# Kernel tuning notes

Hardware: AMD Instinct MI355X
Metric: run time of the kernel (lower is better)

The kernel has to match this reference:

```python
import jax, jax.numpy as jnp
import numpy as np


def setup_inputs() -> dict:
    key = jax.random.key(0)
    k1, k2 = jax.random.split(key)
    B, C, M, N = 4, 3, 4096, 8192
    query = jax.random.normal(k1, (B, C, M), dtype=jnp.float32)
    points = jax.random.normal(k2, (B, C, N), dtype=jnp.float32)
    return {"k": 16, "query": query, "points": points}


def reference(k, query, points):
    # query: BxCxM, points: BxCxN  (trans=True path of original module)
    q = jnp.swapaxes(query, 1, 2)   # BxMxC
    p = jnp.swapaxes(points, 1, 2)  # BxNxC
    # squared L2 distances (FAISS GpuIndexFlatL2): BxMxN
    q2 = jnp.sum(q * q, axis=-1, keepdims=True)           # BxMx1
    p2 = jnp.sum(p * p, axis=-1)[:, None, :]              # Bx1xN
    dist = q2 + p2 - 2.0 * jnp.einsum('bmc,bnc->bmn', q, p)
    # k smallest distances, sorted ascending (FAISS sorts results)
    _, index_batch = jax.lax.top_k(-dist, k)              # BxMxK int32
    index_batch = index_batch.astype(jnp.int64) if index_batch.dtype != jnp.int64 else index_batch
    # gather neighbor coordinates: points BxCxN, idx BxMxK -> BxCxMxK
    neighbor_points = jax.vmap(lambda pts, idx: pts[:, idx])(points, index_batch)
    return neighbor_points, index_batch
```

## Files before the change

kernel.cpp:

```cpp
#include <hip/hip_runtime.h>
#include <stdint.h>

#define BQ 4
#define CC 3
#define MM 4096
#define NN 8192
#define KK 16
#define NP_OFF (BQ*CC*MM*KK)
#define BLOCK 512
#define RPW 8
#define GROUPS 2
#define ROWS 16
#define CHUNK 1024
#define NCH (NN/CHUNK)
#define QST 4
#define EPSD 1e-4f

__device__ __forceinline__ float rfl(float x) {
    return __uint_as_float((unsigned)__builtin_amdgcn_readfirstlane((int)__float_as_uint(x)));
}
__device__ __forceinline__ unsigned mapf(float f) {
    unsigned u = __float_as_uint(f);
    return (u & 0x80000000u) ? ~u : (u | 0x80000000u);
}
__device__ __forceinline__ float unmapf(unsigned u) {
    unsigned b = (u & 0x80000000u) ? (u & 0x7fffffffu) : ~u;
    return __uint_as_float(b);
}

__global__ __launch_bounds__(256) void prep_kernel(
    const float* __restrict__ points, float4* __restrict__ ws4)
{
    int i = blockIdx.x * 256 + threadIdx.x;
    int b = i >> 13, n = i & (NN - 1);
    const float* pb = points + b * (CC * NN);
    float px = pb[n], py = pb[NN + n], pz = pb[2*NN + n];
    float p2 = __fadd_rn(__fadd_rn(__fmul_rn(px,px), __fmul_rn(py,py)),
                         __fmul_rn(pz,pz));
    ws4[i] = make_float4(px, py, pz, -0.5f * p2);
}

__global__ __launch_bounds__(BLOCK, 8) void knn_kernel(
    const float* __restrict__ query,
    const float* __restrict__ points,
    const float4* __restrict__ ws4,
    float* __restrict__ out)
{
    __shared__ float4 pts[2][CHUNK];
    __shared__ unsigned aux[ROWS][64];
    __shared__ unsigned scnt[ROWS];
    __shared__ unsigned rcbits[ROWS];

    const int tid  = threadIdx.x;
    const int lane = tid & 63;
    const int wv   = tid >> 6;
    const int g    = wv >> 2;
    const int qt   = wv & 3;
    const int bid  = blockIdx.x;
    const int b    = bid >> 8;
    const int rb   = (bid & 255) * ROWS;

    const float*  pb  = points + b * (CC * NN);
    const float*  qb  = query  + b * (CC * MM);
    const float4* wsb = ws4 + b * NN;

    ((unsigned*)aux)[tid]       = 0u;
    ((unsigned*)aux)[tid + 512] = 0u;
    if (tid < ROWS) scnt[tid] = 0u;

    float qx[RPW], qy[RPW], qz[RPW], dm[RPW];
    #pragma unroll
    for (int r = 0; r < RPW; ++r) {
        int m = rb + g * RPW + r;
        qx[r] = rfl(qb[m]);
        qy[r] = rfl(qb[MM + m]);
        qz[r] = rfl(qb[2*MM + m]);
        dm[r] = -__builtin_inff();
    }

    float4 pre0, pre1;
    auto loadc = [&](int ch) {
        pre0 = wsb[(ch << 10) + tid];
        pre1 = wsb[(ch << 10) + 512 + tid];
    };
    auto writec = [&](int bi) {
        pts[bi][tid]       = pre0;
        pts[bi][512 + tid] = pre1;
    };

    auto comp1 = [&](int bi) {
        #pragma unroll
        for (int t = 0; t < QST; ++t) {
            float4 P = pts[bi][((qt * QST + t) << 6) + lane];
            #pragma unroll
            for (int r = 0; r < RPW; ++r) {
                float dotf = __builtin_fmaf(qz[r], P.z,
                              __builtin_fmaf(qy[r], P.y,
                               __builtin_fmaf(qx[r], P.x, P.w)));
                dm[r] = fmaxf(dm[r], dotf);
            }
        }
    };

    loadc(0);
    #pragma unroll 1
    for (int ch = 0; ch < NCH; ++ch) {
        int bi = ch & 1;
        writec(bi);
        if (ch + 1 < NCH) loadc(ch + 1);
        if (ch > 0) comp1(bi ^ 1);
        __syncthreads();
    }
    comp1(1);

    #pragma unroll
    for (int r = 0; r < RPW; ++r)
        atomicMax(&aux[g*RPW + r][lane], mapf(dm[r]));
    loadc(0);
    __syncthreads();

    #pragma unroll
    for (int rr = 0; rr < 2; ++rr) {
        int row = 2*wv + rr;
        unsigned v = aux[row][lane];
        #pragma unroll
        for (int k = 2; k <= 64; k <<= 1) {
            #pragma unroll
            for (int j = k >> 1; j > 0; j >>= 1) {
                unsigned o = __shfl_xor(v, j, 64);
                bool keepmin = (((lane & j) == 0) == ((lane & k) == 0));
                v = keepmin ? (v < o ? v : o) : (v > o ? v : o);
            }
        }
        unsigned tb = __shfl(v, 48, 64);
        if (lane == 0) rcbits[row] = __float_as_uint(unmapf(tb) - EPSD);
    }
    __syncthreads();

    float rc[RPW];
    #pragma unroll
    for (int r = 0; r < RPW; ++r)
        rc[r] = rfl(__uint_as_float(rcbits[g*RPW + r]));

    auto comp2 = [&](int ch, int bi) {
        #pragma unroll
        for (int t = 0; t < QST; ++t) {
            int st = qt * QST + t;
            float4 P = pts[bi][(st << 6) + lane];
            unsigned n = (unsigned)((ch << 10) + (st << 6) + lane);
            #pragma unroll
            for (int r = 0; r < RPW; ++r) {
                float dotf = __builtin_fmaf(qz[r], P.z,
                              __builtin_fmaf(qy[r], P.y,
                               __builtin_fmaf(qx[r], P.x, P.w)));
                if (dotf >= rc[r]) {
                    unsigned pos = atomicAdd(&scnt[g*RPW + r], 1u);
                    if (pos < 64u) aux[g*RPW + r][pos] = n;
                }
            }
        }
    };

    comp2(6, 0);
    __syncthreads();
    #pragma unroll 1
    for (int i = 0; i < 6; ++i) {
        writec(i & 1);
        if (i < 5) loadc(i + 1);
        int c = (i == 0) ? 7 : (i - 1);
        comp2(c, c & 1);
        __syncthreads();
    }
    comp2(5, 1);
    __syncthreads();

    #pragma unroll
    for (int rr = 0; rr < 2; ++rr) {
        int row = 2*wv + rr;
        int m   = rb + row;
        float ex = rfl(qb[m]);
        float ey = rfl(qb[MM + m]);
        float ez = rfl(qb[2*MM + m]);
        float eq2 = rfl(__fadd_rn(__fadd_rn(__fmul_rn(ex,ex), __fmul_rn(ey,ey)),
                                  __fmul_rn(ez,ez)));
        unsigned c = scnt[row]; if (c > 64u) c = 64u;
        unsigned kb = 0xffffffffu, id = 0xffffffffu;
        if (lane < (int)c) {
            id = aux[row][lane];
            float px = pb[id], py = pb[NN + id], pz = pb[2*NN + id];
            float p2 = __fadd_rn(__fadd_rn(__fmul_rn(px,px), __fmul_rn(py,py)),
                                 __fmul_rn(pz,pz));
            float dot = __builtin_fmaf(ez, pz,
                         __builtin_fmaf(ey, py, __fmul_rn(ex, px)));
            float d = __fsub_rn(__fadd_rn(eq2, p2), __fmul_rn(2.0f, dot));
            kb = mapf(d);
        }
        #pragma unroll
        for (int k = 2; k <= 64; k <<= 1) {
            #pragma unroll
            for (int j = k >> 1; j > 0; j >>= 1) {
                unsigned ok = __shfl_xor(kb, j, 64);
                unsigned oi = __shfl_xor(id, j, 64);
                bool takeMin  = (((lane & j) == 0) == ((lane & k) == 0));
                bool selfLess = (kb < ok) || (kb == ok && id < oi);
                if (selfLess != takeMin) { kb = ok; id = oi; }
            }
        }
        if (lane < KK) {
            int oi = (int)id;
            out[NP_OFF + (b * MM + m) * KK + lane] = (float)oi;
            out[((b * CC + 0) * MM + m) * KK + lane] = pb[oi];
            out[((b * CC + 1) * MM + m) * KK + lane] = pb[NN + oi];
            out[((b * CC + 2) * MM + m) * KK + lane] = pb[2*NN + oi];
        }
    }
}

extern "C" void kernel_launch(void* const* d_in, const int* in_sizes, int n_in,
                              void* d_out, int out_size, void* d_ws, size_t ws_size,
                              hipStream_t stream) {
    const float* query  = (const float*)d_in[1];
    const float* points = (const float*)d_in[2];
    float4* ws4 = (float4*)d_ws;
    float* out = (float*)d_out;
    prep_kernel<<<dim3((BQ*NN)/256), dim3(256), 0, stream>>>(points, ws4);
    dim3 grid(BQ * (MM / ROWS));
    dim3 block(BLOCK);
    knn_kernel<<<grid, block, 0, stream>>>(query, points, ws4, out);
}
```

Before: 106.5 us.

## Derive kNN threshold from half the points and widen candidate buffer

```diff
diff --git a/kernel.cpp b/kernel.cpp
--- a/kernel.cpp
+++ b/kernel.cpp
@@ -12,9 +12,11 @@
 #define GROUPS 2
 #define ROWS 16
 #define CHUNK 1024
-#define NCH (NN/CHUNK)
+#define NCH 8
+#define SCH 4
 #define QST 4
 #define EPSD 1e-4f
+#define CANDMAX 128
 
 __device__ __forceinline__ float rfl(float x) {
     return __uint_as_float((unsigned)__builtin_amdgcn_readfirstlane((int)__float_as_uint(x)));
@@ -42,7 +44,6 @@
 
 __global__ __launch_bounds__(BLOCK, 8) void knn_kernel(
     const float* __restrict__ query,
-    const float* __restrict__ points,
     const float4* __restrict__ ws4,
     float* __restrict__ out)
 {
@@ -60,8 +61,7 @@
     const int b    = bid >> 8;
     const int rb   = (bid & 255) * ROWS;
 
-    const float*  pb  = points + b * (CC * NN);
-    const float*  qb  = query  + b * (CC * MM);
+    const float*  qb  = query + b * (CC * MM);
     const float4* wsb = ws4 + b * NN;
 
     ((unsigned*)aux)[tid]       = 0u;
@@ -78,14 +78,9 @@
         dm[r] = -__builtin_inff();
     }
 
-    float4 pre0, pre1;
-    auto loadc = [&](int ch) {
-        pre0 = wsb[(ch << 10) + tid];
-        pre1 = wsb[(ch << 10) + 512 + tid];
-    };
-    auto writec = [&](int bi) {
-        pts[bi][tid]       = pre0;
-        pts[bi][512 + tid] = pre1;
+    auto stage = [&](int ch, int bi) {
+        pts[bi][tid]       = wsb[(ch << 10) + tid];
+        pts[bi][512 + tid] = wsb[(ch << 10) + 512 + tid];
     };
 
     auto comp1 = [&](int bi) {
@@ -102,21 +97,20 @@
         }
     };
 
-    loadc(0);
+    stage(0, 0);
     #pragma unroll 1
-    for (int ch = 0; ch < NCH; ++ch) {
-        int bi = ch & 1;
-        writec(bi);
-        if (ch + 1 < NCH) loadc(ch + 1);
-        if (ch > 0) comp1(bi ^ 1);
-        __syncthreads();
-    }
-    comp1(1);
+    for (int ch = 0; ch < SCH; ch += 2) {
+        __syncthreads();
+        if (ch + 1 < SCH) stage(ch + 1, 1);
+        comp1(0);
+        __syncthreads();
+        if (ch + 2 < SCH) stage(ch + 2, 0);
+        if (ch + 1 < SCH) comp1(1);
+    }
 
     #pragma unroll
     for (int r = 0; r < RPW; ++r)
         atomicMax(&aux[g*RPW + r][lane], mapf(dm[r]));
-    loadc(0);
     __syncthreads();
 
     #pragma unroll
@@ -142,6 +136,7 @@
     for (int r = 0; r < RPW; ++r)
         rc[r] = rfl(__uint_as_float(rcbits[g*RPW + r]));
 
+    unsigned short* cbase = (unsigned short*)&aux[0][0];
     auto comp2 = [&](int ch, int bi) {
         #pragma unroll
         for (int t = 0; t < QST; ++t) {
@@ -155,23 +150,29 @@
                                __builtin_fmaf(qx[r], P.x, P.w)));
                 if (dotf >= rc[r]) {
                     unsigned pos = atomicAdd(&scnt[g*RPW + r], 1u);
-                    if (pos < 64u) aux[g*RPW + r][pos] = n;
+                    if (pos < CANDMAX)
+                        cbase[(g*RPW + r) * CANDMAX + pos] = (unsigned short)n;
                 }
             }
         }
     };
 
-    comp2(6, 0);
-    __syncthreads();
+    comp2(2, 0);
+    comp2(3, 1);
+    __syncthreads();
+    stage(0, 0);
     #pragma unroll 1
-    for (int i = 0; i < 6; ++i) {
-        writec(i & 1);
-        if (i < 5) loadc(i + 1);
-        int c = (i == 0) ? 7 : (i - 1);
-        comp2(c, c & 1);
-        __syncthreads();
-    }
-    comp2(5, 1);
+    for (int i = 0; i < 6; i += 2) {
+        int c0 = (i     < 2) ? i     : i + 2;
+        int c1 = (i + 1 < 2) ? i + 1 : i + 3;
+        int c2 = (i + 2 < 2) ? i + 2 : i + 4;
+        __syncthreads();
+        if (i + 1 < 6) stage(c1, 1);
+        comp2(c0, 0);
+        __syncthreads();
+        if (i + 2 < 6) stage(c2, 0);
+        if (i + 1 < 6) comp2(c1, 1);
+    }
     __syncthreads();
 
     #pragma unroll
@@ -183,35 +184,62 @@
         float ez = rfl(qb[2*MM + m]);
         float eq2 = rfl(__fadd_rn(__fadd_rn(__fmul_rn(ex,ex), __fmul_rn(ey,ey)),
                                   __fmul_rn(ez,ez)));
-        unsigned c = scnt[row]; if (c > 64u) c = 64u;
-        unsigned kb = 0xffffffffu, id = 0xffffffffu;
+        unsigned c = scnt[row]; if (c > CANDMAX) c = CANDMAX;
+        const unsigned short* c16 = cbase + row * CANDMAX;
+
+        unsigned kb0 = ~0u, id0 = ~0u, kb1 = ~0u, id1 = ~0u;
         if (lane < (int)c) {
-            id = aux[row][lane];
-            float px = pb[id], py = pb[NN + id], pz = pb[2*NN + id];
-            float p2 = __fadd_rn(__fadd_rn(__fmul_rn(px,px), __fmul_rn(py,py)),
-                                 __fmul_rn(pz,pz));
-            float dot = __builtin_fmaf(ez, pz,
-                         __builtin_fmaf(ey, py, __fmul_rn(ex, px)));
-            float d = __fsub_rn(__fadd_rn(eq2, p2), __fmul_rn(2.0f, dot));
-            kb = mapf(d);
-        }
-        #pragma unroll
-        for (int k = 2; k <= 64; k <<= 1) {
-            #pragma unroll
-            for (int j = k >> 1; j > 0; j >>= 1) {
-                unsigned ok = __shfl_xor(kb, j, 64);
-                unsigned oi = __shfl_xor(id, j, 64);
-                bool takeMin  = (((lane & j) == 0) == ((lane & k) == 0));
-                bool selfLess = (kb < ok) || (kb == ok && id < oi);
-                if (selfLess != takeMin) { kb = ok; id = oi; }
-            }
-        }
+            id0 = c16[lane];
+            float4 P = wsb[id0];
+            float p2  = __fmul_rn(-2.0f, P.w);
+            float dot = __builtin_fmaf(ez, P.z,
+                         __builtin_fmaf(ey, P.y, __fmul_rn(ex, P.x)));
+            kb0 = mapf(__fsub_rn(__fadd_rn(eq2, p2), __fmul_rn(2.0f, dot)));
+        }
+        if (64 + lane < (int)c) {
+            id1 = c16[64 + lane];
+            float4 P = wsb[id1];
+            float p2  = __fmul_rn(-2.0f, P.w);
+            float dot = __builtin_fmaf(ez, P.z,
+                         __builtin_fmaf(ey, P.y, __fmul_rn(ex, P.x)));
+            kb1 = mapf(__fsub_rn(__fadd_rn(eq2, p2), __fmul_rn(2.0f, dot)));
+        }
+
+        auto bsort = [&](unsigned& kb, unsigned& id) {
+            #pragma unroll
+            for (int k = 2; k <= 64; k <<= 1) {
+                #pragma unroll
+                for (int j = k >> 1; j > 0; j >>= 1) {
+                    unsigned ok = __shfl_xor(kb, j, 64);
+                    unsigned oi = __shfl_xor(id, j, 64);
+                    bool takeMin  = (((lane & j) == 0) == ((lane & k) == 0));
+                    bool selfLess = (kb < ok) || (kb == ok && id < oi);
+                    if (selfLess != takeMin) { kb = ok; id = oi; }
+                }
+            }
+        };
+        bsort(kb0, id0);
+        bsort(kb1, id1);
+        unsigned rk = __shfl(kb1, 63 - lane, 64);
+        unsigned ri = __shfl(id1, 63 - lane, 64);
+        bool pLess = (rk < kb0) || (rk == kb0 && ri < id0);
+        if (pLess) { kb0 = rk; id0 = ri; }
+        #pragma unroll
+        for (int j = 32; j > 0; j >>= 1) {
+            unsigned ok = __shfl_xor(kb0, j, 64);
+            unsigned oi = __shfl_xor(id0, j, 64);
+            bool selfLess = (kb0 < ok) || (kb0 == ok && id0 < oi);
+            bool takeMin  = ((lane & j) == 0);
+            if (selfLess != takeMin) { kb0 = ok; id0 = oi; }
+        }
+
         if (lane < KK) {
-            int oi = (int)id;
+            int oi = (int)id0;
+            float4 P = wsb[oi];
             out[NP_OFF + (b * MM + m) * KK + lane] = (float)oi;
-            out[((b * CC + 0) * MM + m) * KK + lane] = pb[oi];
-            out[((b * CC + 1) * MM + m) * KK + lane] = pb[NN + oi];
-            out[((b * CC + 2) * MM + m) * KK + lane] = pb[2*NN + oi];
+            out[((b * CC + 0) * MM + m) * KK + lane] = P.x;
+            out[((b * CC + 1) * MM + m) * KK + lane] = P.y;
+            out[((b * CC + 2) * MM + m) * KK + lane] = P.z;
         }
     }
 }
@@ -226,5 +254,5 @@
     prep_kernel<<<dim3((BQ*NN)/256), dim3(256), 0, stream>>>(points, ws4);
     dim3 grid(BQ * (MM / ROWS));
     dim3 block(BLOCK);
-    knn_kernel<<<grid, block, 0, stream>>>(query, points, ws4, out);
-}
+    knn_kernel<<<grid, block, 0, stream>>>(query, ws4, out);
+}
```

Result: no change. 108.1 us (+1.5%).
